# Performance work log

Hardware: AMD Instinct MI355X
Metric: run time of the kernel (lower is better)

Reference implementation:

```python
import jax, jax.numpy as jnp
import numpy as np


def setup_inputs() -> dict:
    key = jax.random.key(0)
    B, T = 1024, 16384
    n_b, n_a = 2, 2
    u_in = jax.random.normal(key, (B, T), dtype=jnp.float32)
    # initial conditions: y_init[:, i] = y[-1-i], u_init[:, i] = u[-1-i] (scipy lfiltic convention)
    y_init = jnp.zeros((B, n_a), dtype=jnp.float32)
    u_init = jnp.zeros((B, n_b), dtype=jnp.float32)
    # learnable transfer-function coefficients (stable 2nd-order system from the docstring)
    b_coeff = jnp.array([0.0, 0.0706464146944544], dtype=jnp.float32)
    a_coeff = jnp.array([-1.87212998940304, 0.942776404097492], dtype=jnp.float32)
    return {"b_coeff": b_coeff, "a_coeff": a_coeff, "u_in": u_in,
            "y_init": y_init, "u_init": u_init}


def _iir_filter(b_coeff, a_coeff, u_in, y_init, u_init):
    """y[t] = sum_{k=0}^{n_b-1} b_k u[t-k] - sum_{j=1}^{n_a} a_j y[t-j].

    Equivalent to scipy.signal.lfilter(b, [1, *a], u) with initial conditions.
    """
    B, T = u_in.shape
    n_b = b_coeff.shape[0]
    # prepend past inputs in chronological order: u_init[:, i] = u[-1-i]
    u_pad = jnp.concatenate([u_init[:, ::-1], u_in], axis=1)  # (B, n_b + T)
    # feedforward (FIR) part, fully vectorized over B and T
    x = jnp.zeros((B, T), dtype=u_in.dtype)
    for k in range(n_b):  # tiny fixed loop over filter taps
        x = x + b_coeff[k] * jax.lax.dynamic_slice_in_dim(u_pad, n_b - k, T, axis=1)

    # recurrent (IIR) part: carry last n_a outputs, newest first
    def step(yhist, x_t):
        y_t = x_t - yhist @ a_coeff          # (B,)
        yhist = jnp.concatenate([y_t[:, None], yhist[:, :-1]], axis=1)
        return yhist, y_t

    _, y = jax.lax.scan(step, y_init, x.T)   # scan over time; y: (T, B)
    return y.T


def reference(b_coeff, a_coeff, u_in, y_init, u_init):
    return _iir_filter(b_coeff, a_coeff, u_in, y_init, u_init)
```

## Files before the change

kernel.cpp:

```cpp
#include <hip/hip_runtime.h>


constexpr int T_LEN = 16384;
constexpr int LCH   = 64;
constexpr int NCH   = 256;

__device__ __forceinline__ int swz(int t, int q) {
    return t * 16 + (q ^ (t & 15));
}

__global__ __launch_bounds__(NCH) void iir_kernel(
    const float* __restrict__ bco, const float* __restrict__ aco,
    const float* __restrict__ u,   const float* __restrict__ y_init,
    const float* __restrict__ u_init, float* __restrict__ y)
{
    __shared__ float4 lds[T_LEN / 4];
    __shared__ float sh_e1[NCH], sh_e2[NCH];
    __shared__ float sh_s1[NCH], sh_s2[NCH];

    const int row = blockIdx.x;
    const int tid = threadIdx.x;

    const float b0 = bco[0], b1 = bco[1];
    const float a1 = aco[0], a2 = aco[1];

    const float4* __restrict__ u4 = (const float4*)(u + (size_t)row * T_LEN);
    float4* __restrict__ y4       = (float4*)(y + (size_t)row * T_LEN);

    #pragma unroll
    for (int s = 0; s < 16; ++s) {
        const int g = s * 256 + tid;
        const int t = g >> 4, q = g & 15;
        lds[swz(t, q)] = u4[g];
    }
    __syncthreads();

    float u_prev0;
    if (tid == 0) {
        u_prev0 = u_init[2 * row + 0];
    } else {
        const float* ldsf = (const float*)lds;
        u_prev0 = ldsf[swz(tid - 1, 15) * 4 + 3];
    }

#define IIR_STEP(UC, OUTV)                                        \
    {                                                             \
        float x_ = fmaf(b0, (UC), b1 * up);                       \
        (OUTV) = fmaf(-a2, y2, fmaf(-a1, y1, x_));                \
        y2 = y1; y1 = (OUTV); up = (UC);                          \
    }

    float up = u_prev0, y1 = 0.f, y2 = 0.f;
    #pragma unroll
    for (int q = 0; q < 16; ++q) {
        float4 v = lds[swz(tid, q)];
        float t0, t1c, t2c, t3c;
        IIR_STEP(v.x, t0);
        IIR_STEP(v.y, t1c);
        IIR_STEP(v.z, t2c);
        IIR_STEP(v.w, t3c);
        (void)t0; (void)t1c; (void)t2c; (void)t3c;
    }
    sh_e1[tid] = y1;
    sh_e2[tid] = y2;
    __syncthreads();

    if (tid == 0) {
        float pa = 1.f, pb = 0.f;
        #pragma unroll
        for (int k = 0; k <= LCH - 2; ++k) {
            float pn = fmaf(-a2, pb, -(a1 * pa));
            pb = pa; pa = pn;
        }
        const float pL2 = pa, pL3 = pb;
        const float pL1 = fmaf(-a2, pL3, -(a1 * pL2));
        const float qL1 = -a2 * pL2;
        const float qL2 = -a2 * pL3;

        float s1 = y_init[2 * row + 0];
        float s2 = y_init[2 * row + 1];
        for (int c = 0; c < NCH; ++c) {
            sh_s1[c] = s1; sh_s2[c] = s2;
            float n1 = fmaf(qL1, s2, fmaf(pL1, s1, sh_e1[c]));
            float n2 = fmaf(qL2, s2, fmaf(pL2, s1, sh_e2[c]));
            s1 = n1; s2 = n2;
        }
    }
    __syncthreads();

    up = u_prev0;
    y1 = sh_s1[tid];
    y2 = sh_s2[tid];
    #pragma unroll
    for (int q = 0; q < 16; ++q) {
        const int slot = swz(tid, q);
        float4 v = lds[slot];
        float4 o;
        IIR_STEP(v.x, o.x);
        IIR_STEP(v.y, o.y);
        IIR_STEP(v.z, o.z);
        IIR_STEP(v.w, o.w);
        lds[slot] = o;
    }
#undef IIR_STEP
    __syncthreads();

    #pragma unroll
    for (int s = 0; s < 16; ++s) {
        const int g = s * 256 + tid;
        const int t = g >> 4, q = g & 15;
        y4[g] = lds[swz(t, q)];
    }
}

extern "C" void kernel_launch(void* const* d_in, const int* in_sizes, int n_in,
                              void* d_out, int out_size, void* d_ws, size_t ws_size,
                              hipStream_t stream) {
    const float* b  = (const float*)d_in[0];
    const float* a  = (const float*)d_in[1];
    const float* u  = (const float*)d_in[2];
    const float* yi = (const float*)d_in[3];
    const float* ui = (const float*)d_in[4];
    float* yout = (float*)d_out;

    const int B = in_sizes[2] / T_LEN;
    iir_kernel<<<B, NCH, 0, stream>>>(b, a, u, yi, ui, yout);
}
```

Measured before the change: 136.6 us.

## Replace serial chunk-carry scan with wave-shuffle matrix scan over two halves

The kernel now processes each row in two halves of 8192 samples, so the LDS buffer is halved and launch bounds ask for 4 blocks per CU to raise occupancy. The serial 256-step carry propagation on thread 0 is replaced by a parallel prefix scan over 2x2 state-transition matrices. The scan uses warp shuffles within each wave and a short cross-wave combine, with matrix powers precomputed per thread. The costs are more register use for the matrix tables, a sequential dependency between the two halves, and possible numerical differences from the reordered scan.

```diff
diff --git a/kernel.cpp b/kernel.cpp
--- a/kernel.cpp
+++ b/kernel.cpp
@@ -2,45 +2,70 @@
 
 
 constexpr int T_LEN = 16384;
-constexpr int LCH   = 64;
+constexpr int HALF  = 8192;
 constexpr int NCH   = 256;
+constexpr int LCH   = 32;
+constexpr int NQ    = 8;
+constexpr int NSTG  = 8;
 
 __device__ __forceinline__ int swz(int t, int q) {
-    return t * 16 + (q ^ (t & 15));
+    return t * NQ + (q ^ (t & (NQ - 1)));
 }
 
-__global__ __launch_bounds__(NCH) void iir_kernel(
+__global__ __launch_bounds__(NCH, 4) void iir_kernel(
     const float* __restrict__ bco, const float* __restrict__ aco,
     const float* __restrict__ u,   const float* __restrict__ y_init,
     const float* __restrict__ u_init, float* __restrict__ y)
 {
-    __shared__ float4 lds[T_LEN / 4];
-    __shared__ float sh_e1[NCH], sh_e2[NCH];
-    __shared__ float sh_s1[NCH], sh_s2[NCH];
+    __shared__ float4 lds[HALF / 4];
+    __shared__ float sh_wt1[4], sh_wt2[4];
+    __shared__ float sh_carry[3];
 
-    const int row = blockIdx.x;
-    const int tid = threadIdx.x;
+    const int row  = blockIdx.x;
+    const int tid  = threadIdx.x;
+    const int lane = tid & 63;
+    const int wave = tid >> 6;
 
     const float b0 = bco[0], b1 = bco[1];
     const float a1 = aco[0], a2 = aco[1];
 
     const float4* __restrict__ u4 = (const float4*)(u + (size_t)row * T_LEN);
-    float4* __restrict__ y4       = (float4*)(y + (size_t)row * T_LEN);
+    float4*       __restrict__ y4 = (float4*)(y + (size_t)row * T_LEN);
+    const float*  ldsf = (const float*)lds;
+
+    float pa = 1.f, pb = 0.f;
+    #pragma unroll
+    for (int k = 0; k <= LCH - 2; ++k) { float pn = fmaf(-a2, pb, -(a1 * pa)); pb = pa; pa = pn; }
+    const float pL2 = pa, pL3 = pb;
+    const float pL1 = fmaf(-a2, pL3, -(a1 * pL2));
+    float m11[7], m12[7], m21[7], m22[7];
+    m11[0] = pL1; m12[0] = -a2 * pL2; m21[0] = pL2; m22[0] = -a2 * pL3;
+    #pragma unroll
+    for (int k = 1; k < 7; ++k) {
+        m11[k] = fmaf(m11[k-1], m11[k-1], m12[k-1] * m21[k-1]);
+        m12[k] = fmaf(m11[k-1], m12[k-1], m12[k-1] * m22[k-1]);
+        m21[k] = fmaf(m21[k-1], m11[k-1], m22[k-1] * m21[k-1]);
+        m22[k] = fmaf(m21[k-1], m12[k-1], m22[k-1] * m22[k-1]);
+    }
+    float P11 = 1.f, P12 = 0.f, P21 = 0.f, P22 = 1.f;
+    {
+        const int e = lane + 1;
+        #pragma unroll
+        for (int k = 0; k < 7; ++k) {
+            if ((e >> k) & 1) {
+                float n11 = fmaf(m11[k], P11, m12[k] * P21);
+                float n12 = fmaf(m11[k], P12, m12[k] * P22);
+                float n21 = fmaf(m21[k], P11, m22[k] * P21);
+                float n22 = fmaf(m21[k], P12, m22[k] * P22);
+                P11 = n11; P12 = n12; P21 = n21; P22 = n22;
+            }
+        }
+    }
 
     #pragma unroll
-    for (int s = 0; s < 16; ++s) {
-        const int g = s * 256 + tid;
-        const int t = g >> 4, q = g & 15;
-        lds[swz(t, q)] = u4[g];
-    }
-    __syncthreads();
-
-    float u_prev0;
-    if (tid == 0) {
-        u_prev0 = u_init[2 * row + 0];
-    } else {
-        const float* ldsf = (const float*)lds;
-        u_prev0 = ldsf[swz(tid - 1, 15) * 4 + 3];
+    for (int s = 0; s < NSTG; ++s) {
+        const int g = s * NCH + tid;
+        lds[swz(g >> 3, g & 7)] = u4[g];
     }
 
 #define IIR_STEP(UC, OUTV)                                        \
@@ -50,66 +75,91 @@
         y2 = y1; y1 = (OUTV); up = (UC);                          \
     }
 
-    float up = u_prev0, y1 = 0.f, y2 = 0.f;
-    #pragma unroll
-    for (int q = 0; q < 16; ++q) {
-        float4 v = lds[swz(tid, q)];
-        float t0, t1c, t2c, t3c;
-        IIR_STEP(v.x, t0);
-        IIR_STEP(v.y, t1c);
-        IIR_STEP(v.z, t2c);
-        IIR_STEP(v.w, t3c);
-        (void)t0; (void)t1c; (void)t2c; (void)t3c;
-    }
-    sh_e1[tid] = y1;
-    sh_e2[tid] = y2;
-    __syncthreads();
+    #pragma unroll 1
+    for (int h = 0; h < 2; ++h) {
+        __syncthreads();
 
-    if (tid == 0) {
-        float pa = 1.f, pb = 0.f;
+        float up0;
+        if (tid == 0) up0 = (h == 0) ? u_init[2 * row] : sh_carry[2];
+        else          up0 = ldsf[swz(tid - 1, 7) * 4 + 3];
+
+        float up = up0, y1 = 0.f, y2 = 0.f;
         #pragma unroll
-        for (int k = 0; k <= LCH - 2; ++k) {
-            float pn = fmaf(-a2, pb, -(a1 * pa));
-            pb = pa; pa = pn;
+        for (int q = 0; q < NQ; ++q) {
+            float4 v = lds[swz(tid, q)];
+            float t0, t1, t2, t3;
+            IIR_STEP(v.x, t0); IIR_STEP(v.y, t1);
+            IIR_STEP(v.z, t2); IIR_STEP(v.w, t3);
+            (void)t0; (void)t1; (void)t2; (void)t3;
         }
-        const float pL2 = pa, pL3 = pb;
-        const float pL1 = fmaf(-a2, pL3, -(a1 * pL2));
-        const float qL1 = -a2 * pL2;
-        const float qL2 = -a2 * pL3;
+        float v1 = y1, v2 = y2;
+        if (tid == NCH - 1 && h == 0) sh_carry[2] = up;
 
-        float s1 = y_init[2 * row + 0];
-        float s2 = y_init[2 * row + 1];
-        for (int c = 0; c < NCH; ++c) {
-            sh_s1[c] = s1; sh_s2[c] = s2;
-            float n1 = fmaf(qL1, s2, fmaf(pL1, s1, sh_e1[c]));
-            float n2 = fmaf(qL2, s2, fmaf(pL2, s1, sh_e2[c]));
-            s1 = n1; s2 = n2;
+        float s01 = 0.f, s02 = 0.f;
+        if (tid == 0) {
+            s01 = (h == 0) ? y_init[2 * row]     : sh_carry[0];
+            s02 = (h == 0) ? y_init[2 * row + 1] : sh_carry[1];
+            v1 = fmaf(m11[0], s01, fmaf(m12[0], s02, v1));
+            v2 = fmaf(m21[0], s01, fmaf(m22[0], s02, v2));
+        }
+
+        #pragma unroll
+        for (int k = 0; k < 6; ++k) {
+            const int d = 1 << k;
+            float t1 = __shfl_up(v1, d);
+            float t2 = __shfl_up(v2, d);
+            if (lane >= d) {
+                v1 = fmaf(m11[k], t1, fmaf(m12[k], t2, v1));
+                v2 = fmaf(m21[k], t1, fmaf(m22[k], t2, v2));
+            }
+        }
+        if (lane == 63) { sh_wt1[wave] = v1; sh_wt2[wave] = v2; }
+        __syncthreads();
+
+        float q1 = 0.f, q2 = 0.f;
+        for (int w = 0; w < wave; ++w) {
+            float n1 = fmaf(m11[6], q1, fmaf(m12[6], q2, sh_wt1[w]));
+            float n2 = fmaf(m21[6], q1, fmaf(m22[6], q2, sh_wt2[w]));
+            q1 = n1; q2 = n2;
+        }
+        float w1 = fmaf(P11, q1, fmaf(P12, q2, v1));
+        float w2 = fmaf(P21, q1, fmaf(P22, q2, v2));
+        float x1 = __shfl_up(w1, 1);
+        float x2 = __shfl_up(w2, 1);
+        if (lane == 0) { x1 = q1; x2 = q2; }
+        if (tid == 0)  { x1 = s01; x2 = s02; }
+
+        up = up0; y1 = x1; y2 = x2;
+        #pragma unroll
+        for (int q = 0; q < NQ; ++q) {
+            const int slot = swz(tid, q);
+            float4 v = lds[slot];
+            float4 o;
+            IIR_STEP(v.x, o.x); IIR_STEP(v.y, o.y);
+            IIR_STEP(v.z, o.z); IIR_STEP(v.w, o.w);
+            lds[slot] = o;
+        }
+        if (tid == NCH - 1) { sh_carry[0] = y1; sh_carry[1] = y2; }
+        __syncthreads();
+
+        if (h == 0) {
+            #pragma unroll
+            for (int s = 0; s < NSTG; ++s) {
+                const int g = s * NCH + tid;
+                const int slot = swz(g >> 3, g & 7);
+                float4 o = lds[slot];
+                y4[g] = o;
+                float4 v = u4[(HALF / 4) + g];
+                lds[slot] = v;
+            }
         }
     }
-    __syncthreads();
-
-    up = u_prev0;
-    y1 = sh_s1[tid];
-    y2 = sh_s2[tid];
-    #pragma unroll
-    for (int q = 0; q < 16; ++q) {
-        const int slot = swz(tid, q);
-        float4 v = lds[slot];
-        float4 o;
-        IIR_STEP(v.x, o.x);
-        IIR_STEP(v.y, o.y);
-        IIR_STEP(v.z, o.z);
-        IIR_STEP(v.w, o.w);
-        lds[slot] = o;
-    }
 #undef IIR_STEP
-    __syncthreads();
 
     #pragma unroll
-    for (int s = 0; s < 16; ++s) {
-        const int g = s * 256 + tid;
-        const int t = g >> 4, q = g & 15;
-        y4[g] = lds[swz(t, q)];
+    for (int s = 0; s < NSTG; ++s) {
+        const int g = s * NCH + tid;
+        y4[(HALF / 4) + g] = lds[swz(g >> 3, g & 7)];
     }
 }
 
```

New measurement: 123.4 us. -9.7%, faster.
